# Performance work log

Measured on AMD Instinct MI355X. Metric: run time of the kernel, lower is better.

The kernel has to match this reference:

```python
import jax, jax.numpy as jnp
import numpy as np

N_NODES = 50000
N_EDGES = 800000
D_IN = 128
D_OUT = 128


def setup_inputs() -> dict:
    key = jax.random.key(0)
    k1, k2, k3, k4, k5, k6 = jax.random.split(key, 6)
    x = jax.random.normal(k1, (N_NODES, D_IN), dtype=jnp.float32)
    edge_row = jax.random.randint(k2, (N_EDGES,), 0, N_NODES, dtype=jnp.int32)
    edge_col = jax.random.randint(k3, (N_EDGES,), 0, N_NODES, dtype=jnp.int32)
    edge_weight = jax.random.uniform(k4, (N_EDGES,), dtype=jnp.float32)
    W = jax.random.normal(k5, (D_OUT, D_IN), dtype=jnp.float32) * (1.0 / np.sqrt(D_IN))
    b = jax.random.normal(k6, (D_OUT,), dtype=jnp.float32) * 0.01
    return {"x": x, "edge_row": edge_row, "edge_col": edge_col,
            "edge_weight": edge_weight, "W": W, "b": b}


def reference(x, edge_row, edge_col, edge_weight, W, b):
    # SpMM: out[i] = sum_{e: row[e]==i} weight[e] * x[col[e]]
    msgs = edge_weight[:, None] * x[edge_col]            # [E, D_IN]
    agg = jax.ops.segment_sum(msgs, edge_row, num_segments=N_NODES)  # [N, D_IN]
    # nn.Linear: agg @ W.T + b
    return agg @ W.T + b
```

## Files before the change

### kernel.cpp

```cpp
#include <hip/hip_runtime.h>

#define D 128
#define NB_SHIFT 7
#define BKT_NODES 128
#define PB 128
#define MAXB 400
#define S2CAP 3072

typedef __attribute__((ext_vector_type(8))) short bf16x8;
typedef __attribute__((ext_vector_type(4))) float f32x4;

__device__ __forceinline__ short f2bf_rne(float f) {
  unsigned u = __float_as_uint(f);
  unsigned r = u + 0x7fffu + ((u >> 16) & 1u);
  return (short)(r >> 16);
}

__device__ __forceinline__ bf16x8 pack_bf16x8(float4 a, float4 b) {
  bf16x8 h;
  h[0] = f2bf_rne(a.x); h[1] = f2bf_rne(a.y);
  h[2] = f2bf_rne(a.z); h[3] = f2bf_rne(a.w);
  h[4] = f2bf_rne(b.x); h[5] = f2bf_rne(b.y);
  h[6] = f2bf_rne(b.z); h[7] = f2bf_rne(b.w);
  return h;
}

__global__ __launch_bounds__(256) void bhist_kernel(const int* __restrict__ erow,
                                                    int* __restrict__ h,
                                                    int* __restrict__ gbcnt,
                                                    int E, int B) {
  __shared__ int lh[MAXB];
  for (int i = threadIdx.x; i < B; i += 256) lh[i] = 0;
  __syncthreads();
  const int chunk = (E + PB - 1) / PB;
  const int begin = blockIdx.x * chunk;
  const int end = min(begin + chunk, E);
  for (int e = begin + threadIdx.x; e < end; e += 256)
    atomicAdd(&lh[erow[e] >> NB_SHIFT], 1);
  __syncthreads();
  for (int i = threadIdx.x; i < B; i += 256) {
    int v = lh[i];
    h[blockIdx.x * MAXB + i] = v;
    if (v) atomicAdd(&gbcnt[i], v);
  }
}

__global__ __launch_bounds__(512) void bscan_kernel(const int* __restrict__ gbcnt,
                                                    int* __restrict__ bstart,
                                                    int* __restrict__ gcur, int B) {
  __shared__ int lds[512];
  const int t = threadIdx.x;
  int v = (t < B) ? gbcnt[t] : 0;
  lds[t] = v;
  __syncthreads();
  for (int off = 1; off < 512; off <<= 1) {
    int u = (t >= off) ? lds[t - off] : 0;
    __syncthreads();
    if (t >= off) lds[t] += u;
    __syncthreads();
  }
  if (t < B) {
    int excl = lds[t] - v;
    bstart[t] = excl;
    gcur[t] = excl;
  }
}

__global__ __launch_bounds__(256) void part_gemm_kernel(
    const int* __restrict__ erow, const int* __restrict__ ecol,
    const float* __restrict__ ew, const int* __restrict__ h,
    int* __restrict__ gcur, int2* __restrict__ swcol,
    const float* __restrict__ x, const float* __restrict__ W,
    ushort* __restrict__ y, int E, int N, int B) {
  __shared__ int lcur[MAXB];

  if (blockIdx.x < PB) {
    const int tid = threadIdx.x;
    for (int i = tid; i < B; i += 256) {
      int v = h[blockIdx.x * MAXB + i];
      lcur[i] = v ? atomicAdd(&gcur[i], v) : 0;
    }
    __syncthreads();
    const int chunk = (E + PB - 1) / PB;
    const int begin = blockIdx.x * chunk;
    const int end = min(begin + chunk, E);
    for (int e = begin + tid; e < end; e += 256) {
      int r = erow[e];
      int bkt = r >> NB_SHIFT;
      int rl = r & (BKT_NODES - 1);
      int pos = atomicAdd(&lcur[bkt], 1);
      swcol[pos] = make_int2((rl << 16) | ecol[e], __float_as_int(ew[e]));
    }
  } else {
    const int tid = threadIdx.x;
    const int wave = tid >> 6, lane = tid & 63;
    const int m_half = wave & 1;
    const int n_half = wave >> 1;
    const int l16 = lane & 15, quad = lane >> 4;

    bf16x8 Bf[4][4];
    const float4* W4 = (const float4*)W;
#pragma unroll
    for (int nt = 0; nt < 4; ++nt) {
      int n = n_half * 64 + nt * 16 + l16;
#pragma unroll
      for (int kb = 0; kb < 4; ++kb) {
        int idx = (n * D + kb * 32 + quad * 8) >> 2;
        Bf[nt][kb] = pack_bf16x8(W4[idx], W4[idx + 1]);
      }
    }

    const float4* x4 = (const float4*)x;
    const int ntiles = (N + 63) >> 6;
    const int gstride = gridDim.x - PB;
    for (int tile = (int)blockIdx.x - PB; tile < ntiles; tile += gstride) {
      const int row0 = tile * 64 + m_half * 32;
      f32x4 acc[2][4];
#pragma unroll
      for (int mt = 0; mt < 2; ++mt)
#pragma unroll
        for (int nt = 0; nt < 4; ++nt)
          acc[mt][nt] = (f32x4){0.f, 0.f, 0.f, 0.f};

#pragma unroll
      for (int kb = 0; kb < 4; ++kb) {
        const int k0 = kb * 32 + quad * 8;
        int m0 = row0 + l16;      if (m0 > N - 1) m0 = N - 1;
        int m1 = row0 + 16 + l16; if (m1 > N - 1) m1 = N - 1;
        int i0 = (m0 * D + k0) >> 2;
        int i1 = (m1 * D + k0) >> 2;
        float4 p0 = x4[i0], q0 = x4[i0 + 1];
        float4 p1 = x4[i1], q1 = x4[i1 + 1];
        bf16x8 a0 = pack_bf16x8(p0, q0);
        bf16x8 a1 = pack_bf16x8(p1, q1);
#pragma unroll
        for (int nt = 0; nt < 4; ++nt) {
          acc[0][nt] = __builtin_amdgcn_mfma_f32_16x16x32_bf16(a0, Bf[nt][kb], acc[0][nt], 0, 0, 0);
          acc[1][nt] = __builtin_amdgcn_mfma_f32_16x16x32_bf16(a1, Bf[nt][kb], acc[1][nt], 0, 0, 0);
        }
      }

#pragma unroll
      for (int mt = 0; mt < 2; ++mt) {
        int rbase = row0 + mt * 16 + quad * 4;
#pragma unroll
        for (int nt = 0; nt < 4; ++nt) {
          int col = n_half * 64 + nt * 16 + l16;
#pragma unroll
          for (int r = 0; r < 4; ++r) {
            int row = rbase + r;
            if (row < N) y[row * D + col] = (ushort)f2bf_rne(acc[mt][nt][r]);
          }
        }
      }
    }
  }
}

__global__ __launch_bounds__(256) void stage2_kernel(
    const int2* __restrict__ swcol, int2* __restrict__ swcol2,
    const int* __restrict__ bstart, const int* __restrict__ gbcnt,
    int* __restrict__ startN, int* __restrict__ cntN, int N) {
  __shared__ int2 ebuf[S2CAP];
  __shared__ int nh[BKT_NODES], sc[BKT_NODES], ncur[BKT_NODES];
  const int b = blockIdx.x, tid = threadIdx.x;
  const int s = bstart[b];
  const int c = gbcnt[b];
  const bool lds_path = (c <= S2CAP);

  if (tid < BKT_NODES) nh[tid] = 0;
  if (lds_path)
    for (int j = tid; j < c; j += 256) ebuf[j] = swcol[s + j];
  __syncthreads();

  if (lds_path) {
    for (int j = tid; j < c; j += 256) atomicAdd(&nh[ebuf[j].x >> 16], 1);
  } else {
    for (int j = tid; j < c; j += 256) atomicAdd(&nh[swcol[s + j].x >> 16], 1);
  }
  __syncthreads();

  if (tid < BKT_NODES) sc[tid] = nh[tid];
  __syncthreads();
  for (int off = 1; off < BKT_NODES; off <<= 1) {
    int v = 0;
    if (tid < BKT_NODES && tid >= off) v = sc[tid - off];
    __syncthreads();
    if (tid < BKT_NODES && tid >= off) sc[tid] += v;
    __syncthreads();
  }
  if (tid < BKT_NODES) {
    int excl = sc[tid] - nh[tid];
    ncur[tid] = excl;
    int node = (b << NB_SHIFT) + tid;
    if (node < N) { startN[node] = s + excl; cntN[node] = nh[tid]; }
  }
  __syncthreads();

  if (lds_path) {
    for (int j = tid; j < c; j += 256) {
      int2 en = ebuf[j];
      int pos = atomicAdd(&ncur[en.x >> 16], 1);
      swcol2[s + pos] = en;
    }
  } else {
    for (int j = tid; j < c; j += 256) {
      int2 en = swcol[s + j];
      int pos = atomicAdd(&ncur[en.x >> 16], 1);
      swcol2[s + pos] = en;
    }
  }
}

__global__ __launch_bounds__(256) void gather_agg_kernel(
    const ushort* __restrict__ y, const int* __restrict__ startN,
    const int* __restrict__ cntN, const int2* __restrict__ swcol2,
    const float* __restrict__ bias, float* __restrict__ out, int N) {
  const int node = blockIdx.x * 4 + (threadIdx.x >> 6);
  const int lane = threadIdx.x & 63;
  if (node >= N) return;

  const unsigned* __restrict__ y1 = (const unsigned*)y;
  float2 acc = ((const float2*)bias)[lane];

  const int s = startN[node];
  const int t = s + cntN[node];
#pragma unroll 4
  for (int j = s; j < t; ++j) {
    int2 cw = swcol2[j];
    int col = cw.x & 0xFFFF;
    float wg = __int_as_float(cw.y);
    unsigned v = y1[col * 64 + lane];
    float f0 = __uint_as_float(v << 16);
    float f1 = __uint_as_float(v & 0xffff0000u);
    acc.x += wg * f0;
    acc.y += wg * f1;
  }
  ((float2*)out)[node * 64 + lane] = acc;
}

extern "C" void kernel_launch(void* const* d_in, const int* in_sizes, int n_in,
                              void* d_out, int out_size, void* d_ws, size_t ws_size,
                              hipStream_t stream) {
  const float* x    = (const float*)d_in[0];
  const int*   erow = (const int*)d_in[1];
  const int*   ecol = (const int*)d_in[2];
  const float* ew   = (const float*)d_in[3];
  const float* W    = (const float*)d_in[4];
  const float* b    = (const float*)d_in[5];
  float* out = (float*)d_out;

  const int N = in_sizes[0] / D;
  const int E = in_sizes[1];
  const int B = (N + BKT_NODES - 1) >> NB_SHIFT;

  char* ws = (char*)d_ws;
  ushort* y      = (ushort*)ws;
  int2*   swcol  = (int2*)(ws + (size_t)N * D * 2);
  int2*   swcol2 = swcol + E;
  int*    h      = (int*)(swcol2 + E);
  int*    gbcnt  = h + PB * MAXB;
  int*    bstart = gbcnt + MAXB;
  int*    gcur   = bstart + MAXB;
  int*    startN = gcur + MAXB;
  int*    cntN   = startN + N;

  hipMemsetAsync(gbcnt, 0, (size_t)B * sizeof(int), stream);

  bhist_kernel<<<PB, 256, 0, stream>>>(erow, h, gbcnt, E, B);
  bscan_kernel<<<1, 512, 0, stream>>>(gbcnt, bstart, gcur, B);

  const int ntiles = (N + 63) >> 6;
  part_gemm_kernel<<<PB + ntiles, 256, 0, stream>>>(
      erow, ecol, ew, h, gcur, swcol, x, W, y, E, N, B);

  stage2_kernel<<<B, 256, 0, stream>>>(swcol, swcol2, bstart, gbcnt, startN, cntN, N);

  gather_agg_kernel<<<(N + 3) / 4, 256, 0, stream>>>(y, startN, cntN, swcol2, b, out, N);
}
```

Baseline: 172.1 us.

## Fuse bucket sort with gather aggregation and precompute per-block write offsets

Merges the per-bucket node sort and the neighbor gather into one kernel that sorts edges in LDS and aggregates directly, removing the swcol2/startN/cntN round trip and two launches. Bucket totals and per-partition write windows are computed in the scan kernel from the histogram, replacing global atomics and the memset. Gather parallelism falls to one block per 128-node bucket with large LDS use, which may reduce latency hiding for random y reads; oversize buckets use a slow quadratic fallback.

```diff
diff --git a/kernel.cpp b/kernel.cpp
--- a/kernel.cpp
+++ b/kernel.cpp
@@ -27,7 +27,6 @@
 
 __global__ __launch_bounds__(256) void bhist_kernel(const int* __restrict__ erow,
                                                     int* __restrict__ h,
-                                                    int* __restrict__ gbcnt,
                                                     int E, int B) {
   __shared__ int lh[MAXB];
   for (int i = threadIdx.x; i < B; i += 256) lh[i] = 0;
@@ -38,19 +37,21 @@
   for (int e = begin + threadIdx.x; e < end; e += 256)
     atomicAdd(&lh[erow[e] >> NB_SHIFT], 1);
   __syncthreads();
-  for (int i = threadIdx.x; i < B; i += 256) {
-    int v = lh[i];
-    h[blockIdx.x * MAXB + i] = v;
-    if (v) atomicAdd(&gbcnt[i], v);
-  }
-}
-
-__global__ __launch_bounds__(512) void bscan_kernel(const int* __restrict__ gbcnt,
+  for (int i = threadIdx.x; i < B; i += 256)
+    h[blockIdx.x * MAXB + i] = lh[i];
+}
+
+__global__ __launch_bounds__(512) void bscan_kernel(const int* __restrict__ h,
+                                                    int* __restrict__ gbcnt,
                                                     int* __restrict__ bstart,
-                                                    int* __restrict__ gcur, int B) {
+                                                    int* __restrict__ wwin, int B) {
   __shared__ int lds[512];
   const int t = threadIdx.x;
-  int v = (t < B) ? gbcnt[t] : 0;
+  int v = 0;
+  if (t < B) {
+#pragma unroll 8
+    for (int bb = 0; bb < PB; ++bb) v += h[bb * MAXB + t];
+  }
   lds[t] = v;
   __syncthreads();
   for (int off = 1; off < 512; off <<= 1) {
@@ -61,25 +62,29 @@
   }
   if (t < B) {
     int excl = lds[t] - v;
+    gbcnt[t] = v;
     bstart[t] = excl;
-    gcur[t] = excl;
+    int run = excl;
+#pragma unroll 8
+    for (int bb = 0; bb < PB; ++bb) {
+      wwin[bb * MAXB + t] = run;
+      run += h[bb * MAXB + t];
+    }
   }
 }
 
 __global__ __launch_bounds__(256) void part_gemm_kernel(
     const int* __restrict__ erow, const int* __restrict__ ecol,
-    const float* __restrict__ ew, const int* __restrict__ h,
-    int* __restrict__ gcur, int2* __restrict__ swcol,
+    const float* __restrict__ ew, const int* __restrict__ wwin,
+    int2* __restrict__ swcol,
     const float* __restrict__ x, const float* __restrict__ W,
     ushort* __restrict__ y, int E, int N, int B) {
   __shared__ int lcur[MAXB];
 
   if (blockIdx.x < PB) {
     const int tid = threadIdx.x;
-    for (int i = tid; i < B; i += 256) {
-      int v = h[blockIdx.x * MAXB + i];
-      lcur[i] = v ? atomicAdd(&gcur[i], v) : 0;
-    }
+    for (int i = tid; i < B; i += 256)
+      lcur[i] = wwin[blockIdx.x * MAXB + i];
     __syncthreads();
     const int chunk = (E + PB - 1) / PB;
     const int begin = blockIdx.x * chunk;
@@ -157,86 +162,80 @@
   }
 }
 
-__global__ __launch_bounds__(256) void stage2_kernel(
-    const int2* __restrict__ swcol, int2* __restrict__ swcol2,
-    const int* __restrict__ bstart, const int* __restrict__ gbcnt,
-    int* __restrict__ startN, int* __restrict__ cntN, int N) {
+__global__ __launch_bounds__(256) void sort_gather_kernel(
+    const int2* __restrict__ swcol, const int* __restrict__ bstart,
+    const int* __restrict__ gbcnt, const ushort* __restrict__ y,
+    const float* __restrict__ bias, float* __restrict__ out, int N) {
   __shared__ int2 ebuf[S2CAP];
+  __shared__ int2 ebuf2[S2CAP];
   __shared__ int nh[BKT_NODES], sc[BKT_NODES], ncur[BKT_NODES];
+
   const int b = blockIdx.x, tid = threadIdx.x;
   const int s = bstart[b];
   const int c = gbcnt[b];
-  const bool lds_path = (c <= S2CAP);
-
-  if (tid < BKT_NODES) nh[tid] = 0;
-  if (lds_path)
+  const int wave = tid >> 6, lane = tid & 63;
+  const unsigned* __restrict__ y1 = (const unsigned*)y;
+  const float2 bv = ((const float2*)bias)[lane];
+
+  if (c <= S2CAP) {
+    if (tid < BKT_NODES) nh[tid] = 0;
     for (int j = tid; j < c; j += 256) ebuf[j] = swcol[s + j];
-  __syncthreads();
-
-  if (lds_path) {
+    __syncthreads();
     for (int j = tid; j < c; j += 256) atomicAdd(&nh[ebuf[j].x >> 16], 1);
-  } else {
-    for (int j = tid; j < c; j += 256) atomicAdd(&nh[swcol[s + j].x >> 16], 1);
-  }
-  __syncthreads();
-
-  if (tid < BKT_NODES) sc[tid] = nh[tid];
-  __syncthreads();
-  for (int off = 1; off < BKT_NODES; off <<= 1) {
-    int v = 0;
-    if (tid < BKT_NODES && tid >= off) v = sc[tid - off];
-    __syncthreads();
-    if (tid < BKT_NODES && tid >= off) sc[tid] += v;
-    __syncthreads();
-  }
-  if (tid < BKT_NODES) {
-    int excl = sc[tid] - nh[tid];
-    ncur[tid] = excl;
-    int node = (b << NB_SHIFT) + tid;
-    if (node < N) { startN[node] = s + excl; cntN[node] = nh[tid]; }
-  }
-  __syncthreads();
-
-  if (lds_path) {
+    __syncthreads();
+    if (tid < BKT_NODES) sc[tid] = nh[tid];
+    __syncthreads();
+    for (int off = 1; off < BKT_NODES; off <<= 1) {
+      int v = 0;
+      if (tid < BKT_NODES && tid >= off) v = sc[tid - off];
+      __syncthreads();
+      if (tid < BKT_NODES && tid >= off) sc[tid] += v;
+      __syncthreads();
+    }
+    if (tid < BKT_NODES) ncur[tid] = sc[tid] - nh[tid];
+    __syncthreads();
     for (int j = tid; j < c; j += 256) {
       int2 en = ebuf[j];
       int pos = atomicAdd(&ncur[en.x >> 16], 1);
-      swcol2[s + pos] = en;
+      ebuf2[pos] = en;
+    }
+    __syncthreads();
+
+    for (int i = 0; i < 32; ++i) {
+      int rl = wave * 32 + i;
+      int node = (b << NB_SHIFT) + rl;
+      if (node >= N) continue;
+      int e1 = sc[rl];
+      int e0 = e1 - nh[rl];
+      float2 acc = bv;
+#pragma unroll 4
+      for (int j = e0; j < e1; ++j) {
+        int2 en = ebuf2[j];
+        float wg = __int_as_float(en.y);
+        unsigned v = y1[(en.x & 0xFFFF) * 64 + lane];
+        acc.x += wg * __uint_as_float(v << 16);
+        acc.y += wg * __uint_as_float(v & 0xffff0000u);
+      }
+      ((float2*)out)[node * 64 + lane] = acc;
     }
   } else {
-    for (int j = tid; j < c; j += 256) {
-      int2 en = swcol[s + j];
-      int pos = atomicAdd(&ncur[en.x >> 16], 1);
-      swcol2[s + pos] = en;
-    }
-  }
-}
-
-__global__ __launch_bounds__(256) void gather_agg_kernel(
-    const ushort* __restrict__ y, const int* __restrict__ startN,
-    const int* __restrict__ cntN, const int2* __restrict__ swcol2,
-    const float* __restrict__ bias, float* __restrict__ out, int N) {
-  const int node = blockIdx.x * 4 + (threadIdx.x >> 6);
-  const int lane = threadIdx.x & 63;
-  if (node >= N) return;
-
-  const unsigned* __restrict__ y1 = (const unsigned*)y;
-  float2 acc = ((const float2*)bias)[lane];
-
-  const int s = startN[node];
-  const int t = s + cntN[node];
-#pragma unroll 4
-  for (int j = s; j < t; ++j) {
-    int2 cw = swcol2[j];
-    int col = cw.x & 0xFFFF;
-    float wg = __int_as_float(cw.y);
-    unsigned v = y1[col * 64 + lane];
-    float f0 = __uint_as_float(v << 16);
-    float f1 = __uint_as_float(v & 0xffff0000u);
-    acc.x += wg * f0;
-    acc.y += wg * f1;
-  }
-  ((float2*)out)[node * 64 + lane] = acc;
+    for (int i = 0; i < 32; ++i) {
+      int rl = wave * 32 + i;
+      int node = (b << NB_SHIFT) + rl;
+      if (node >= N) continue;
+      float2 acc = bv;
+      for (int j = 0; j < c; ++j) {
+        int2 en = swcol[s + j];
+        if ((en.x >> 16) == rl) {
+          float wg = __int_as_float(en.y);
+          unsigned v = y1[(en.x & 0xFFFF) * 64 + lane];
+          acc.x += wg * __uint_as_float(v << 16);
+          acc.y += wg * __uint_as_float(v & 0xffff0000u);
+        }
+      }
+      ((float2*)out)[node * 64 + lane] = acc;
+    }
+  }
 }
 
 extern "C" void kernel_launch(void* const* d_in, const int* in_sizes, int n_in,
@@ -257,24 +256,17 @@
   char* ws = (char*)d_ws;
   ushort* y      = (ushort*)ws;
   int2*   swcol  = (int2*)(ws + (size_t)N * D * 2);
-  int2*   swcol2 = swcol + E;
-  int*    h      = (int*)(swcol2 + E);
-  int*    gbcnt  = h + PB * MAXB;
+  int*    h      = (int*)(swcol + E);
+  int*    wwin   = h + PB * MAXB;
+  int*    gbcnt  = wwin + PB * MAXB;
   int*    bstart = gbcnt + MAXB;
-  int*    gcur   = bstart + MAXB;
-  int*    startN = gcur + MAXB;
-  int*    cntN   = startN + N;
-
-  hipMemsetAsync(gbcnt, 0, (size_t)B * sizeof(int), stream);
-
-  bhist_kernel<<<PB, 256, 0, stream>>>(erow, h, gbcnt, E, B);
-  bscan_kernel<<<1, 512, 0, stream>>>(gbcnt, bstart, gcur, B);
+
+  bhist_kernel<<<PB, 256, 0, stream>>>(erow, h, E, B);
+  bscan_kernel<<<1, 512, 0, stream>>>(h, gbcnt, bstart, wwin, B);
 
   const int ntiles = (N + 63) >> 6;
   part_gemm_kernel<<<PB + ntiles, 256, 0, stream>>>(
-      erow, ecol, ew, h, gcur, swcol, x, W, y, E, N, B);
-
-  stage2_kernel<<<B, 256, 0, stream>>>(swcol, swcol2, bstart, gbcnt, startN, cntN, N);
-
-  gather_agg_kernel<<<(N + 3) / 4, 256, 0, stream>>>(y, startN, cntN, swcol2, b, out, N);
-}
+      erow, ecol, ew, wwin, swcol, x, W, y, E, N, B);
+
+  sort_gather_kernel<<<B, 256, 0, stream>>>(swcol, bstart, gbcnt, y, b, out, N);
+}
```

Result: slower. 208.5 us (+21.2%).
